# Kernel optimization log

Measured on AMD Instinct MI355X. Metric: run time of the kernel, lower is better.

## Reference

```python
import jax, jax.numpy as jnp
import numpy as np

N = 8192          # number of priors
TOP_K = 50        # max detections returned
IOU_THR = 0.3     # NMS IoU threshold (module-level constant)
VAR0, VAR1 = 0.1, 0.2  # variance buffer


def setup_inputs() -> dict:
    key = jax.random.key(0)
    k1, k2, k3, k4, k5 = jax.random.split(key, 5)
    loc = jax.random.normal(k1, (N, 14), jnp.float32)
    conf = jax.random.uniform(k2, (N, 2), jnp.float32)
    # some iou scores slightly out of [0,1] to exercise the clamp
    iou = jax.random.uniform(k3, (N, 1), jnp.float32) * 1.2 - 0.1
    cxcy = jax.random.uniform(k4, (N, 2), jnp.float32)            # anchor centers in [0,1)
    wh = jax.random.uniform(k5, (N, 2), jnp.float32) * 0.19 + 0.01  # anchor sizes in (0.01,0.2)
    priors = jnp.concatenate([cxcy, wh], axis=1)
    return {"loc": loc, "conf": conf, "iou": iou, "priors": priors}


def _decode(loc, conf, iou, priors):
    cls_scores = conf[:, 1]
    iou_scores = jnp.clip(iou[:, 0], 0.0, 1.0)
    scores = jnp.sqrt(cls_scores * iou_scores)
    p_cxcy, p_wh = priors[:, 0:2], priors[:, 2:4]
    bb_cxcy = p_cxcy + loc[:, 0:2] * VAR0 * p_wh
    var = jnp.array([VAR0, VAR1], jnp.float32)
    bb_wh_half = p_wh * jnp.exp(loc[:, 2:4] * var) * 0.5
    bboxes = jnp.concatenate([bb_cxcy - bb_wh_half, bb_cxcy + bb_wh_half], axis=1)
    # 5 landmarks, each decoded like the box center
    lms = jnp.concatenate(
        [p_cxcy + loc[:, 4 + 2 * i:6 + 2 * i] * VAR0 * p_wh for i in range(5)], axis=1)
    return bboxes, lms, scores


def _nms_keep_idx(bboxes, scores):
    """Greedy NMS; returns indices (into original order) of the first TOP_K kept boxes."""
    order = jnp.argsort(-scores)
    b = bboxes[order]
    x1, y1, x2, y2 = b[:, 0], b[:, 1], b[:, 2], b[:, 3]
    area = (x2 - x1) * (y2 - y1)
    iw = jnp.maximum(jnp.minimum(x2[:, None], x2[None, :]) - jnp.maximum(x1[:, None], x1[None, :]), 0.0)
    ih = jnp.maximum(jnp.minimum(y2[:, None], y2[None, :]) - jnp.maximum(y1[:, None], y1[None, :]), 0.0)
    inter = iw * ih
    iou_mat = inter / (area[:, None] + area[None, :] - inter)  # [N, N]
    idxs = jnp.arange(N)

    def body(i, keep):
        suppressed = jnp.any((iou_mat[i] > IOU_THR) & keep & (idxs < i))
        return keep.at[i].set(~suppressed)

    keep = jax.lax.fori_loop(0, N, body, jnp.zeros((N,), bool))
    kept_pos = jnp.nonzero(keep, size=TOP_K, fill_value=0)[0]  # fixed-size under jit
    return order[kept_pos]


def reference(loc, conf, iou, priors):
    bboxes, lms, scores = _decode(loc, conf, iou, priors)
    keep_idx = _nms_keep_idx(bboxes, scores)
    dets = jnp.concatenate(
        [bboxes[keep_idx], lms[keep_idx], scores[keep_idx][:, None]], axis=1)  # [TOP_K, 15]
    return dets
```

## Files before the change

kernel.cpp:

```cpp
#include <hip/hip_runtime.h>

#define NBOX 8192
#define TOP_K 50
#define IOU_THR 0.3f
#define VAR0 0.1f
#define VAR1 0.2f
#define NT 512
#define NWAVE (NT / 64)
#define MSEL 128
#define PRE_MAX 256
#define BPT 16

__device__ __forceinline__ void decode_box(int cidx, const float* __restrict__ loc,
                                           const float* __restrict__ priors,
                                           float& x1, float& y1, float& x2, float& y2,
                                           float& area)
{
    float4 pr = *reinterpret_cast<const float4*>(priors + 4 * cidx);
    float l0 = loc[cidx * 14 + 0];
    float l1 = loc[cidx * 14 + 1];
    float l2 = loc[cidx * 14 + 2];
    float l3 = loc[cidx * 14 + 3];
    float cx = pr.x + l0 * VAR0 * pr.z;
    float cy = pr.y + l1 * VAR0 * pr.w;
    float hw = pr.z * expf(l2 * VAR0) * 0.5f;
    float hh = pr.w * expf(l3 * VAR1) * 0.5f;
    x1 = cx - hw; y1 = cy - hh; x2 = cx + hw; y2 = cy + hh;
    area = (x2 - x1) * (y2 - y1);
}

__device__ __forceinline__ void find_thresh(unsigned c0, unsigned c1, unsigned c2, unsigned c3,
                                            int lane, int& bin_sel)
{
    unsigned cnt = c0 + c1 + c2 + c3;
    unsigned S = cnt;
    #pragma unroll
    for (int d = 1; d < 64; d <<= 1) {
        unsigned t = __shfl_down(S, d);
        if (lane + d < 64) S += t;
    }
    unsigned long long bal = __ballot(S >= MSEL);
    int lstar = 63 - __clzll(bal);
    int src = (lstar < 63) ? (lstar + 1) : lstar;
    unsigned Snext = __shfl(S, src);
    unsigned above = (lstar < 63) ? Snext : 0u;
    unsigned bl[4] = {c0, c1, c2, c3};
    int bsel = -1; unsigned acc = above;
    #pragma unroll
    for (int k = 3; k >= 0; --k) {
        if (bsel < 0) {
            if (acc + bl[k] >= MSEL) bsel = k;
            else acc += bl[k];
        }
    }
    bin_sel = 4 * lstar + __shfl(bsel, lstar);
}

__device__ void bitonic_sort(unsigned long long* a, int S, int tid)
{
    for (int k = 2; k <= S; k <<= 1) {
        for (int j = k >> 1; j > 0; j >>= 1) {
            __syncthreads();
            for (int i = tid; i < S; i += NT) {
                int l = i ^ j;
                if (l > i) {
                    unsigned long long A = a[i];
                    unsigned long long B = a[l];
                    bool asc = ((i & k) == 0);
                    if ((A > B) == asc) { a[i] = B; a[l] = A; }
                }
            }
        }
    }
    __syncthreads();
}

__device__ void greedy_nms_serial(const unsigned long long* __restrict__ arr, int n, int lane,
                                  const float* __restrict__ loc, const float* __restrict__ priors,
                                  int* keep_out)
{
    float kx1 = 0.f, ky1 = 0.f, kx2 = 0.f, ky2 = 0.f, karea = 0.f;
    int my_keep = 0, idx0 = 0, kept = 0;
    bool done = false;
    for (int p = 0; p < n && !done; p += 64) {
        int cidx = 0;
        float x1 = 0.f, y1 = 0.f, x2 = 0.f, y2 = 0.f, area = 0.f;
        int pos = p + lane;
        if (pos < n) {
            cidx = (int)(arr[pos] & 0xFFFFFFFFull);
            decode_box(cidx, loc, priors, x1, y1, x2, y2, area);
        }
        int nb = (n - p) < 64 ? (n - p) : 64;
        for (int c = 0; c < nb; ++c) {
            float bx1 = __shfl(x1, c);
            float by1 = __shfl(y1, c);
            float bx2 = __shfl(x2, c);
            float by2 = __shfl(y2, c);
            float barea = __shfl(area, c);
            int   bidx  = __shfl(cidx, c);
            float iw = fmaxf(fminf(kx2, bx2) - fmaxf(kx1, bx1), 0.0f);
            float ih = fmaxf(fminf(ky2, by2) - fmaxf(ky1, by1), 0.0f);
            float inter = iw * ih;
            float v = inter / (karea + barea - inter);
            bool sup = (lane < kept) && (v > IOU_THR);
            if (__ballot(sup) == 0ull) {
                if (kept == 0) idx0 = bidx;
                if (lane == kept) {
                    kx1 = bx1; ky1 = by1; kx2 = bx2; ky2 = by2; karea = barea;
                    my_keep = bidx;
                }
                ++kept;
                if (kept == TOP_K) { done = true; break; }
            }
        }
    }
    if (lane < TOP_K) keep_out[lane] = (lane < kept) ? my_keep : idx0;
}

__global__ __launch_bounds__(NT) void yunet_fused_kernel(
    const float* __restrict__ loc,
    const float* __restrict__ conf,
    const float* __restrict__ iou,
    const float* __restrict__ priors,
    float* __restrict__ out)
{
    __shared__ unsigned long long keys[NBOX];
    __shared__ unsigned long long cand[PRE_MAX];
    __shared__ unsigned hist[NWAVE][256] __attribute__((aligned(16)));
    __shared__ unsigned long long maskbuf[64];
    __shared__ unsigned long long sh_supprev;
    __shared__ float4 boxs4[PRE_MAX];
    __shared__ float  boxsa[PRE_MAX];
    __shared__ int    idxs[PRE_MAX];
    __shared__ float4 keptb4[TOP_K];
    __shared__ float  kepta[TOP_K];
    __shared__ int keep_sh[TOP_K];
    __shared__ unsigned sh_cnt;
    __shared__ int sh_flag, sh_kept;

    const int tid  = threadIdx.x;
    const int lane = tid & 63;
    const int wid  = tid >> 6;

    const float4* conf4 = reinterpret_cast<const float4*>(conf);
    const float4* iou4  = reinterpret_cast<const float4*>(iou);
    float4 cf[8], io[4];
    #pragma unroll
    for (int m = 0; m < 2; ++m)
        #pragma unroll
        for (int q = 0; q < 4; ++q)
            cf[m * 4 + q] = conf4[(m * NT + tid) * 4 + q];
    #pragma unroll
    for (int m = 0; m < 2; ++m)
        #pragma unroll
        for (int r = 0; r < 2; ++r)
            io[m * 2 + r] = iou4[(m * NT + tid) * 2 + r];

    #pragma unroll
    for (int i = 0; i < 4; ++i) hist[wid][lane + 64 * i] = 0;
    if (tid == 0) { sh_cnt = 0; sh_flag = 0; sh_kept = 0; }
    __asm__ volatile("s_waitcnt lgkmcnt(0)" ::: "memory");

    unsigned sbv[BPT];
    #pragma unroll
    for (int m = 0; m < 2; ++m) {
        float sc[8], uu[8];
        #pragma unroll
        for (int q = 0; q < 4; ++q) {
            sc[2 * q]     = cf[m * 4 + q].y;
            sc[2 * q + 1] = cf[m * 4 + q].w;
        }
        #pragma unroll
        for (int r = 0; r < 2; ++r) {
            uu[4 * r + 0] = io[m * 2 + r].x; uu[4 * r + 1] = io[m * 2 + r].y;
            uu[4 * r + 2] = io[m * 2 + r].z; uu[4 * r + 3] = io[m * 2 + r].w;
        }
        #pragma unroll
        for (int q = 0; q < 8; ++q) {
            float u = fminf(fmaxf(uu[q], 0.0f), 1.0f);
            float s = sqrtf(sc[q] * u);
            unsigned sb = __float_as_uint(s);
            sbv[m * 8 + q] = sb;
            int bin = (int)(s * 256.0f); bin = bin > 255 ? 255 : bin;
            atomicAdd(&hist[wid][bin], 1u);
        }
    }
    __syncthreads();

    int B;
    {
        unsigned c0 = 0, c1 = 0, c2 = 0, c3 = 0;
        #pragma unroll
        for (int w = 0; w < NWAVE; ++w) {
            uint4 h = *(const uint4*)&hist[w][4 * lane];
            c0 += h.x; c1 += h.y; c2 += h.z; c3 += h.w;
        }
        find_thresh(c0, c1, c2, c3, lane, B);
    }

    #pragma unroll
    for (int m = 0; m < 2; ++m) {
        #pragma unroll
        for (int q = 0; q < 8; ++q) {
            unsigned sb = sbv[m * 8 + q];
            float s = __uint_as_float(sb);
            int bin = (int)(s * 256.0f); bin = bin > 255 ? 255 : bin;
            bool pred = (bin >= B);
            unsigned long long bal = __ballot(pred);
            if (pred) {
                int myoff = __popcll(bal & ((1ull << lane) - 1ull));
                unsigned base = 0;
                if (myoff == 0) base = atomicAdd(&sh_cnt, (unsigned)__popcll(bal));
                base = (unsigned)__builtin_amdgcn_readfirstlane((int)base);
                unsigned pos = base + (unsigned)myoff;
                if (pos < PRE_MAX)
                    cand[pos] = ((unsigned long long)(~sb) << 32)
                              | (unsigned)((m * NT + tid) * 8 + q);
            }
        }
    }
    __syncthreads();
    const int C = (int)sh_cnt;

    if (C <= PRE_MAX) {
        if (tid < C) {
            unsigned long long k = cand[tid];
            int r = 0, j = 0;
            for (; j + 4 <= C; j += 4) {
                r += (cand[j]     < k) ? 1 : 0;
                r += (cand[j + 1] < k) ? 1 : 0;
                r += (cand[j + 2] < k) ? 1 : 0;
                r += (cand[j + 3] < k) ? 1 : 0;
            }
            for (; j < C; ++j) r += (cand[j] < k) ? 1 : 0;
            int cidx = (int)(k & 0xFFFFFFFFull);
            float x1, y1, x2, y2, area;
            decode_box(cidx, loc, priors, x1, y1, x2, y2, area);
            boxs4[r] = make_float4(x1, y1, x2, y2);
            boxsa[r] = area;
            idxs[r] = cidx;
        }
        __syncthreads();

        for (int p = 0; p < C; p += 64) {
            if (tid < 64) {
                int pos = p + lane;
                bool valid = pos < C;
                int rp = valid ? pos : 0;
                float4 b = boxs4[rp]; float a = boxsa[rp];
                int kept = sh_kept;
                bool supP = !valid;
                for (int j = 0; j < kept; ++j) {
                    float4 kb = keptb4[j]; float ka = kepta[j];
                    float iw = fmaxf(fminf(b.z, kb.z) - fmaxf(b.x, kb.x), 0.f);
                    float ih = fmaxf(fminf(b.w, kb.w) - fmaxf(b.y, kb.y), 0.f);
                    float inter = iw * ih;
                    supP = supP || (inter > IOU_THR * (a + ka - inter));
                }
                unsigned long long sp = __ballot(supP);
                if (lane == 0) sh_supprev = sp;
            }
            {
                int r  = tid >> 3;
                int cb = tid & 7;
                int rp = (p + r < C) ? p + r : 0;
                float4 rb = boxs4[rp]; float ra = boxsa[rp];
                unsigned byte = 0;
                #pragma unroll
                for (int k = 0; k < 8; ++k) {
                    int c = cb * 8 + k;
                    int cp = (p + c < C) ? p + c : 0;
                    float4 cx = boxs4[cp]; float ca = boxsa[cp];
                    float iw = fmaxf(fminf(rb.z, cx.z) - fmaxf(rb.x, cx.x), 0.f);
                    float ih = fmaxf(fminf(rb.w, cx.w) - fmaxf(rb.y, cx.y), 0.f);
                    float inter = iw * ih;
                    byte |= (unsigned)((inter > IOU_THR * (ra + ca - inter)) ? 1u : 0u) << k;
                }
                ((unsigned char*)maskbuf)[tid] = (unsigned char)byte;
            }
            __syncthreads();

            if (tid < 64) {
                unsigned long long mymask = maskbuf[lane];
                unsigned long long sup_prev = sh_supprev;
                unsigned long long keepcur = 0ull;
                const int kept0 = sh_kept;
                int kept = kept0;
                for (int i2 = 0; i2 < 64 && kept < TOP_K; ++i2) {
                    unsigned long long mi = __shfl(mymask, i2);
                    unsigned long long lower = (1ull << i2) - 1ull;
                    if (!((sup_prev >> i2) & 1ull) && !(mi & keepcur & lower)) {
                        keepcur |= 1ull << i2;
                        ++kept;
                    }
                }
                unsigned long long lowm = (1ull << lane) - 1ull;
                int rank = kept0 + __popcll(keepcur & lowm);
                if (((keepcur >> lane) & 1ull) && rank < TOP_K) {
                    int pos = p + lane;
                    keep_sh[rank] = idxs[pos];
                    keptb4[rank] = boxs4[pos];
                    kepta[rank] = boxsa[pos];
                }
                if (lane == 0) sh_kept = kept;
            }
            __syncthreads();
            if (sh_kept >= TOP_K) break;
        }
        if (tid == 0) sh_flag = (sh_kept >= TOP_K) ? 0 : 1;
    } else {
        if (tid == 0) sh_flag = 1;
    }
    __syncthreads();

    if (sh_flag) {
        #pragma unroll
        for (int m = 0; m < 2; ++m) {
            #pragma unroll
            for (int q = 0; q < 8; ++q) {
                int i = (m * NT + tid) * 8 + q;
                keys[i] = ((unsigned long long)(~sbv[m * 8 + q]) << 32) | (unsigned)i;
            }
        }
        __syncthreads();
        bitonic_sort(keys, NBOX, tid);
        if (tid < 64) greedy_nms_serial(keys, NBOX, tid, loc, priors, keep_sh);
        if (tid == 0) sh_kept = TOP_K;
        __syncthreads();
    }

    if (tid < TOP_K) {
        int src = (tid < sh_kept) ? tid : 0;
        int i = keep_sh[src];
        float4 pr = *reinterpret_cast<const float4*>(priors + 4 * i);
        float cx = pr.x + loc[i * 14 + 0] * VAR0 * pr.z;
        float cy = pr.y + loc[i * 14 + 1] * VAR0 * pr.w;
        float hw = pr.z * expf(loc[i * 14 + 2] * VAR0) * 0.5f;
        float hh = pr.w * expf(loc[i * 14 + 3] * VAR1) * 0.5f;
        float* o = out + tid * 15;
        o[0] = cx - hw;
        o[1] = cy - hh;
        o[2] = cx + hw;
        o[3] = cy + hh;
        #pragma unroll
        for (int q = 0; q < 5; ++q) {
            o[4 + 2 * q] = pr.x + loc[i * 14 + 4 + 2 * q] * VAR0 * pr.z;
            o[5 + 2 * q] = pr.y + loc[i * 14 + 5 + 2 * q] * VAR0 * pr.w;
        }
        float cc = conf[i * 2 + 1];
        float u  = fminf(fmaxf(iou[i], 0.0f), 1.0f);
        o[14] = sqrtf(cc * u);
    }
}

extern "C" void kernel_launch(void* const* d_in, const int* in_sizes, int n_in,
                              void* d_out, int out_size, void* d_ws, size_t ws_size,
                              hipStream_t stream) {
    const float* loc    = (const float*)d_in[0];
    const float* conf   = (const float*)d_in[1];
    const float* iou    = (const float*)d_in[2];
    const float* priors = (const float*)d_in[3];
    float* out = (float*)d_out;

    yunet_fused_kernel<<<1, NT, 0, stream>>>(loc, conf, iou, priors, out);
}
```

Baseline: 23.60 us.

## Build score histogram from a quarter sample and streamline block NMS loop

The threshold histogram is now built from only every fourth score, with the selection target scaled down to match. This cuts the shared-memory atomic traffic by about three quarters. The greedy NMS loop now keeps the suppression ballot and kept count in registers instead of shared variables, reads mask rows with readlane, and skips rows that are already suppressed. The fallback flag and its extra barrier are removed. The risk is that the sampled threshold is less accurate, which can yield too few or too many candidates and send the kernel into the costly full bitonic-sort fallback.

```diff
diff --git a/kernel.cpp b/kernel.cpp
--- a/kernel.cpp
+++ b/kernel.cpp
@@ -7,7 +7,7 @@
 #define VAR1 0.2f
 #define NT 512
 #define NWAVE (NT / 64)
-#define MSEL 128
+#define MSEL_SUB 32
 #define PRE_MAX 256
 #define BPT 16
 
@@ -30,7 +30,7 @@
 }
 
 __device__ __forceinline__ void find_thresh(unsigned c0, unsigned c1, unsigned c2, unsigned c3,
-                                            int lane, int& bin_sel)
+                                            int lane, unsigned target, int& bin_sel)
 {
     unsigned cnt = c0 + c1 + c2 + c3;
     unsigned S = cnt;
@@ -39,7 +39,7 @@
         unsigned t = __shfl_down(S, d);
         if (lane + d < 64) S += t;
     }
-    unsigned long long bal = __ballot(S >= MSEL);
+    unsigned long long bal = __ballot(S >= target);
     int lstar = 63 - __clzll(bal);
     int src = (lstar < 63) ? (lstar + 1) : lstar;
     unsigned Snext = __shfl(S, src);
@@ -49,7 +49,7 @@
     #pragma unroll
     for (int k = 3; k >= 0; --k) {
         if (bsel < 0) {
-            if (acc + bl[k] >= MSEL) bsel = k;
+            if (acc + bl[k] >= target) bsel = k;
             else acc += bl[k];
         }
     }
@@ -128,7 +128,6 @@
     __shared__ unsigned long long cand[PRE_MAX];
     __shared__ unsigned hist[NWAVE][256] __attribute__((aligned(16)));
     __shared__ unsigned long long maskbuf[64];
-    __shared__ unsigned long long sh_supprev;
     __shared__ float4 boxs4[PRE_MAX];
     __shared__ float  boxsa[PRE_MAX];
     __shared__ int    idxs[PRE_MAX];
@@ -136,7 +135,7 @@
     __shared__ float  kepta[TOP_K];
     __shared__ int keep_sh[TOP_K];
     __shared__ unsigned sh_cnt;
-    __shared__ int sh_flag, sh_kept;
+    __shared__ int sh_kept;
 
     const int tid  = threadIdx.x;
     const int lane = tid & 63;
@@ -158,7 +157,7 @@
 
     #pragma unroll
     for (int i = 0; i < 4; ++i) hist[wid][lane + 64 * i] = 0;
-    if (tid == 0) { sh_cnt = 0; sh_flag = 0; sh_kept = 0; }
+    if (tid == 0) { sh_cnt = 0; sh_kept = 0; }
     __asm__ volatile("s_waitcnt lgkmcnt(0)" ::: "memory");
 
     unsigned sbv[BPT];
@@ -181,8 +180,10 @@
             float s = sqrtf(sc[q] * u);
             unsigned sb = __float_as_uint(s);
             sbv[m * 8 + q] = sb;
-            int bin = (int)(s * 256.0f); bin = bin > 255 ? 255 : bin;
-            atomicAdd(&hist[wid][bin], 1u);
+            if ((q & 3) == 0) {
+                int bin = (int)(s * 256.0f); bin = bin > 255 ? 255 : bin;
+                atomicAdd(&hist[wid][bin], 1u);
+            }
         }
     }
     __syncthreads();
@@ -195,7 +196,7 @@
             uint4 h = *(const uint4*)&hist[w][4 * lane];
             c0 += h.x; c1 += h.y; c2 += h.z; c3 += h.w;
         }
-        find_thresh(c0, c1, c2, c3, lane, B);
+        find_thresh(c0, c1, c2, c3, lane, MSEL_SUB, B);
     }
 
     #pragma unroll
@@ -222,7 +223,8 @@
     __syncthreads();
     const int C = (int)sh_cnt;
 
-    if (C <= PRE_MAX) {
+    bool main_ok = (C <= PRE_MAX);
+    if (main_ok) {
         if (tid < C) {
             unsigned long long k = cand[tid];
             int r = 0, j = 0;
@@ -242,23 +244,23 @@
         }
         __syncthreads();
 
+        int kept_reg = 0;
         for (int p = 0; p < C; p += 64) {
+            unsigned long long sup_prev = 0ull;
             if (tid < 64) {
                 int pos = p + lane;
                 bool valid = pos < C;
                 int rp = valid ? pos : 0;
                 float4 b = boxs4[rp]; float a = boxsa[rp];
-                int kept = sh_kept;
                 bool supP = !valid;
-                for (int j = 0; j < kept; ++j) {
+                for (int j = 0; j < kept_reg; ++j) {
                     float4 kb = keptb4[j]; float ka = kepta[j];
                     float iw = fmaxf(fminf(b.z, kb.z) - fmaxf(b.x, kb.x), 0.f);
                     float ih = fmaxf(fminf(b.w, kb.w) - fmaxf(b.y, kb.y), 0.f);
                     float inter = iw * ih;
                     supP = supP || (inter > IOU_THR * (a + ka - inter));
                 }
-                unsigned long long sp = __ballot(supP);
-                if (lane == 0) sh_supprev = sp;
+                sup_prev = __ballot(supP);
             }
             {
                 int r  = tid >> 3;
@@ -281,39 +283,40 @@
             __syncthreads();
 
             if (tid < 64) {
-                unsigned long long mymask = maskbuf[lane];
-                unsigned long long sup_prev = sh_supprev;
+                unsigned long long myrow = maskbuf[lane];
+                unsigned mlo = (unsigned)myrow;
+                unsigned mhi = (unsigned)(myrow >> 32);
                 unsigned long long keepcur = 0ull;
-                const int kept0 = sh_kept;
+                const int kept0 = kept_reg;
                 int kept = kept0;
-                for (int i2 = 0; i2 < 64 && kept < TOP_K; ++i2) {
-                    unsigned long long mi = __shfl(mymask, i2);
-                    unsigned long long lower = (1ull << i2) - 1ull;
-                    if (!((sup_prev >> i2) & 1ull) && !(mi & keepcur & lower)) {
-                        keepcur |= 1ull << i2;
-                        ++kept;
+                for (int j = 0; j < 64 && kept < TOP_K; ++j) {
+                    if (!((sup_prev >> j) & 1ull)) {
+                        unsigned long long mj =
+                            ((unsigned long long)(unsigned)__builtin_amdgcn_readlane((int)mhi, j) << 32)
+                          | (unsigned)__builtin_amdgcn_readlane((int)mlo, j);
+                        unsigned long long lower = (1ull << j) - 1ull;
+                        if (!(mj & keepcur & lower)) { keepcur |= 1ull << j; ++kept; }
                     }
                 }
                 unsigned long long lowm = (1ull << lane) - 1ull;
-                int rank = kept0 + __popcll(keepcur & lowm);
-                if (((keepcur >> lane) & 1ull) && rank < TOP_K) {
+                if ((keepcur >> lane) & 1ull) {
+                    int rank = kept0 + __popcll(keepcur & lowm);
                     int pos = p + lane;
                     keep_sh[rank] = idxs[pos];
                     keptb4[rank] = boxs4[pos];
                     kepta[rank] = boxsa[pos];
                 }
+                kept_reg = kept;
                 if (lane == 0) sh_kept = kept;
             }
             __syncthreads();
             if (sh_kept >= TOP_K) break;
         }
-        if (tid == 0) sh_flag = (sh_kept >= TOP_K) ? 0 : 1;
-    } else {
-        if (tid == 0) sh_flag = 1;
-    }
-    __syncthreads();
-
-    if (sh_flag) {
+    }
+    const int kept_total = main_ok ? sh_kept : 0;
+    const bool need_fallback = (kept_total < TOP_K);
+
+    if (need_fallback) {
         #pragma unroll
         for (int m = 0; m < 2; ++m) {
             #pragma unroll
@@ -325,12 +328,12 @@
         __syncthreads();
         bitonic_sort(keys, NBOX, tid);
         if (tid < 64) greedy_nms_serial(keys, NBOX, tid, loc, priors, keep_sh);
-        if (tid == 0) sh_kept = TOP_K;
         __syncthreads();
     }
+    const int kcnt = need_fallback ? TOP_K : kept_total;
 
     if (tid < TOP_K) {
-        int src = (tid < sh_kept) ? tid : 0;
+        int src = (tid < kcnt) ? tid : 0;
         int i = keep_sh[src];
         float4 pr = *reinterpret_cast<const float4*>(priors + 4 * i);
         float cx = pr.x + loc[i * 14 + 0] * VAR0 * pr.z;
```

Result: faster. 22.77 us (median of 2 runs) (-3.5%).
